# Kernel optimization log

Hardware: AMD Instinct MI355X
Metric: run time of the kernel (lower is better)

## Reference

```python
import jax, jax.numpy as jnp
import numpy as np

N = 50000          # num nodes
E = 800000         # num edges
H, C = 2, 64       # heads, per-head channels (hidden_dim=64)
IN_DIM = 128
EDGE_DIM = 32
NEG_SLOPE = 0.2


def setup_inputs() -> dict:
    key = jax.random.key(0)
    ks = jax.random.split(key, 20)
    s = 0.05
    inp = {
        'x': jax.random.normal(ks[0], (N, IN_DIM), jnp.float32),
        'edge_index': jax.random.randint(ks[1], (2, E), 0, N, jnp.int64),
        'edge_attr': jax.random.normal(ks[2], (E, EDGE_DIM), jnp.float32),
    }
    k = 3
    for l in range(3):
        inp[f'Wl{l}'] = jax.random.normal(ks[k], (IN_DIM, H * C), jnp.float32) * s; k += 1
        inp[f'Wr{l}'] = jax.random.normal(ks[k], (IN_DIM, H * C), jnp.float32) * s; k += 1
        inp[f'We{l}'] = jax.random.normal(ks[k], (EDGE_DIM, H * C), jnp.float32) * s; k += 1
        inp[f'att{l}'] = jax.random.normal(ks[k], (H, C), jnp.float32) * s; k += 1
        inp[f'b{l}'] = jnp.zeros((H * C,), jnp.float32)
    return inp


def gatv2_layer(x, src, dst, edge_attr, Wl, Wr, We, att, b):
    # PyG GATv2Conv (concat=True, share_weights=False):
    #   e_ij = att . LeakyReLU(Wl x_j + Wr x_i + We edge_ij)
    #   alpha = softmax_j over neighborhood of dst i; out_i = sum_j alpha_ij * (Wl x_j)
    xl = (x @ Wl).reshape(-1, H, C)              # [N,H,C] source transform
    xr = (x @ Wr).reshape(-1, H, C)              # [N,H,C] target transform
    ea = (edge_attr @ We).reshape(-1, H, C)      # [E,H,C]
    xj = xl[src]                                 # [E,H,C] gather source
    e = jax.nn.leaky_relu(xj + xr[dst] + ea, NEG_SLOPE)
    logits = jnp.einsum('ehc,hc->eh', e, att)    # [E,H]
    # segment softmax over dst neighborhoods
    m = jax.ops.segment_max(logits, dst, num_segments=N)  # [N,H]
    m = jnp.where(jnp.isfinite(m), m, 0.0)
    ex = jnp.exp(logits - m[dst])
    denom = jax.ops.segment_sum(ex, dst, num_segments=N)  # [N,H]
    alpha = ex / (denom[dst] + 1e-16)            # [E,H]
    out = jax.ops.segment_sum(alpha[:, :, None] * xj, dst, num_segments=N)  # [N,H,C]
    return out.reshape(-1, H * C) + b


def reference(x, edge_index, edge_attr,
              Wl0, Wr0, We0, att0, b0,
              Wl1, Wr1, We1, att1, b1,
              Wl2, Wr2, We2, att2, b2):
    src, dst = edge_index[0], edge_index[1]
    h = gatv2_layer(x, src, dst, edge_attr, Wl0, Wr0, We0, att0, b0)
    h = jax.nn.relu(h)
    h = gatv2_layer(h, src, dst, edge_attr, Wl1, Wr1, We1, att1, b1)
    h = jax.nn.relu(h)
    h = gatv2_layer(h, src, dst, edge_attr, Wl2, Wr2, We2, att2, b2)
    return h
```

## Files before the change

### kernel.cpp

```cpp
#include <hip/hip_runtime.h>

typedef unsigned int u32;
typedef unsigned short u16;
typedef __attribute__((ext_vector_type(8))) short bf16x8;
typedef __attribute__((ext_vector_type(4))) float f32x4;

__device__ __forceinline__ u16 f2b(float f){
  u32 x = __float_as_uint(f);
  u32 r = (x + 0x7fffu + ((x >> 16) & 1u)) >> 16;
  return (u16)r;
}
__device__ __forceinline__ float b2f(u16 h){ return __uint_as_float((u32)h << 16); }
__device__ __forceinline__ float bl(u32 u){ return __uint_as_float(u << 16); }
__device__ __forceinline__ float bh(u32 u){ return __uint_as_float(u & 0xffff0000u); }


__global__ void k_detect(const u32* __restrict__ ei, int n, u32* __restrict__ flag){
  int t = blockIdx.x * blockDim.x + threadIdx.x;
  u32 v = 0;
  if (t < n) v = ei[2 * t + 1];
  unsigned long long b = __ballot(v != 0u);
  if ((threadIdx.x & 63) == 0 && b) atomicOr(flag, 1u);
}

__global__ void k_convhist(const int* __restrict__ ei, int* __restrict__ src, int* __restrict__ dst,
                           int* __restrict__ deg, const float* __restrict__ eattr,
                           u16* __restrict__ ea2, int E, const u32* __restrict__ flag){
  int e = blockIdx.x * blockDim.x + threadIdx.x;
  if (e >= E) return;
  bool is64 = (*flag == 0u);
  int s, d;
  if (is64){ s = ei[2 * e]; d = ei[2 * (E + e)]; }
  else     { s = ei[e];     d = ei[E + e]; }
  src[e] = s; dst[e] = d;
  atomicAdd(&deg[d], 1);
  const float4* srow = (const float4*)(eattr + (size_t)e * 32);
  u32 pk[16];
  #pragma unroll
  for (int i = 0; i < 8; i++){
    float4 v = srow[i];
    pk[2*i]   = (u32)f2b(v.x) | ((u32)f2b(v.y) << 16);
    pk[2*i+1] = (u32)f2b(v.z) | ((u32)f2b(v.w) << 16);
  }
  uint4* drow = (uint4*)(ea2 + (size_t)e * 32);
  drow[0] = make_uint4(pk[0], pk[1], pk[2], pk[3]);
  drow[1] = make_uint4(pk[4], pk[5], pk[6], pk[7]);
  drow[2] = make_uint4(pk[8], pk[9], pk[10], pk[11]);
  drow[3] = make_uint4(pk[12], pk[13], pk[14], pk[15]);
}

__global__ __launch_bounds__(256) void k_scan1(const int* __restrict__ deg, int* __restrict__ bsum, int n){
  int b = blockIdx.x, t = threadIdx.x, lane = t & 63, wv = t >> 6;
  int i0 = b * 1024 + t * 4;
  int4 v = make_int4(0,0,0,0);
  if (i0 + 3 < n) v = *(const int4*)(deg + i0);
  else { if (i0 < n) v.x = deg[i0]; if (i0+1 < n) v.y = deg[i0+1]; if (i0+2 < n) v.z = deg[i0+2]; }
  int s = v.x + v.y + v.z + v.w;
  #pragma unroll
  for (int off = 1; off < 64; off <<= 1) s += __shfl_xor(s, off);
  __shared__ int ws[4];
  if (lane == 0) ws[wv] = s;
  __syncthreads();
  if (t == 0) bsum[b] = ws[0] + ws[1] + ws[2] + ws[3];
}

__global__ __launch_bounds__(1024) void k_scan2(int* __restrict__ bsum, int nb, int* __restrict__ segN){
  int t = threadIdx.x, lane = t & 63, w = t >> 6;
  int v = (t < nb) ? bsum[t] : 0;
  int x = v;
  #pragma unroll
  for (int off = 1; off < 64; off <<= 1){
    int y = __shfl_up(x, off);
    if (lane >= off) x += y;
  }
  __shared__ int wsum[16];
  if (lane == 63) wsum[w] = x;
  __syncthreads();
  if (w == 0 && lane < 16){
    int sv = wsum[lane];
    #pragma unroll
    for (int off = 1; off < 16; off <<= 1){
      int y = __shfl_up(sv, off);
      if (lane >= off) sv += y;
    }
    wsum[lane] = sv;
  }
  __syncthreads();
  int woff = (w > 0) ? wsum[w - 1] : 0;
  if (t < nb) bsum[t] = woff + x - v;
  if (t == 0) *segN = wsum[15];
}

__global__ __launch_bounds__(256) void k_scan3(const int* __restrict__ deg, const int* __restrict__ bsum,
                                               int* __restrict__ seg, int n){
  int b = blockIdx.x, t = threadIdx.x, lane = t & 63, wv = t >> 6;
  int i0 = b * 1024 + t * 4;
  int4 v = make_int4(0,0,0,0);
  if (i0 + 3 < n) v = *(const int4*)(deg + i0);
  else { if (i0 < n) v.x = deg[i0]; if (i0+1 < n) v.y = deg[i0+1]; if (i0+2 < n) v.z = deg[i0+2]; }
  int s = v.x + v.y + v.z + v.w;
  int x = s;
  #pragma unroll
  for (int off = 1; off < 64; off <<= 1){
    int y = __shfl_up(x, off);
    if (lane >= off) x += y;
  }
  __shared__ int ws[4];
  if (lane == 63) ws[wv] = x;
  __syncthreads();
  int woff = 0;
  #pragma unroll
  for (int k = 0; k < 4; k++) if (k < wv) woff += ws[k];
  int base = bsum[b] + woff + (x - s);
  if (i0 < n)     seg[i0]     = base;
  if (i0+1 < n)   seg[i0+1]   = base + v.x;
  if (i0+2 < n)   seg[i0+2]   = base + v.x + v.y;
  if (i0+3 < n)   seg[i0+3]   = base + v.x + v.y + v.z;
}

__global__ void k_scatter(const int* __restrict__ src, const int* __restrict__ dst,
                          const int* __restrict__ seg, int* __restrict__ cur,
                          int* __restrict__ ssrc, int* __restrict__ sdst,
                          int* __restrict__ seid, int E){
  int e = blockIdx.x * blockDim.x + threadIdx.x;
  if (e >= E) return;
  int d = dst[e];
  int pos = seg[d] + atomicAdd(&cur[d], 1);
  ssrc[pos] = src[e];
  sdst[pos] = d;
  seid[pos] = e;
}

__global__ __launch_bounds__(256) void k_prepw(
    const float* __restrict__ W0, const float* __restrict__ W1, const float* __restrict__ W2,
    const float* __restrict__ W3, const float* __restrict__ W4, const float* __restrict__ W5,
    u16* __restrict__ WtH, u16* __restrict__ WtL)
{
  int mat = blockIdx.z;
  const float* W = (mat == 0) ? W0 : (mat == 1) ? W1 : (mat == 2) ? W2 :
                   (mat == 3) ? W3 : (mat == 4) ? W4 : W5;
  __shared__ float tile[32][33];
  int kt = blockIdx.x * 32, ct = blockIdx.y * 32;
  int tr = threadIdx.x & 31, ti = threadIdx.x >> 5;
  #pragma unroll
  for (int j = 0; j < 4; j++){
    int kk = ti + 8 * j;
    tile[kk][tr] = W[(size_t)(kt + kk) * 128 + ct + tr];
  }
  __syncthreads();
  #pragma unroll
  for (int j = 0; j < 4; j++){
    int cc = ti + 8 * j;
    float v = tile[tr][cc];
    u16 hi = f2b(v);
    u16 lo = f2b(v - b2f(hi));
    size_t o = (size_t)mat * 16384 + (size_t)(ct + cc) * 128 + kt + tr;
    WtH[o] = hi;
    WtL[o] = lo;
  }
}

__global__ __launch_bounds__(256) void k_gemm2(
    const float* __restrict__ A,
    const u16* __restrict__ WtH, const u16* __restrict__ WtL,
    u16* __restrict__ xlb, u16* __restrict__ xrb, int nrows)
{
  __shared__ u16 sAH[64][72], sAL[64][72];
  __shared__ u16 sWH[128][72], sWL[128][72];
  int t = threadIdx.x, wv = t >> 6, lane = t & 63;
  int col = lane & 15, kg = lane >> 4;
  int r0 = blockIdx.x * 64;
  int mat = blockIdx.y;
  const u16* WHb = WtH + (size_t)mat * 16384;
  const u16* WLb = WtL + (size_t)mat * 16384;

  f32x4 acc[4][2];
  #pragma unroll
  for (int m = 0; m < 4; m++)
    #pragma unroll
    for (int n = 0; n < 2; n++)
      acc[m][n] = (f32x4){0.f, 0.f, 0.f, 0.f};

  int ar = t >> 2, ak = (t & 3) << 4;
  int wc = t >> 1, wk = (t & 1) << 5;

  for (int kh = 0; kh < 2; kh++){
    __syncthreads();
    {
      int gr = r0 + ar;
      const float* ap = A + (size_t)gr * 128 + kh * 64 + ak;
      float4 va = {0,0,0,0}, vb = {0,0,0,0}, vc = {0,0,0,0}, vd = {0,0,0,0};
      if (gr < nrows){
        va = *(const float4*)ap; vb = *(const float4*)(ap + 4);
        vc = *(const float4*)(ap + 8); vd = *(const float4*)(ap + 12);
      }
      float fv[16] = { va.x, va.y, va.z, va.w, vb.x, vb.y, vb.z, vb.w,
                       vc.x, vc.y, vc.z, vc.w, vd.x, vd.y, vd.z, vd.w };
      u32 hp[8], lp[8];
      #pragma unroll
      for (int i = 0; i < 8; i++){
        u16 h0 = f2b(fv[2*i]),   h1 = f2b(fv[2*i+1]);
        u16 l0 = f2b(fv[2*i]   - b2f(h0));
        u16 l1 = f2b(fv[2*i+1] - b2f(h1));
        hp[i] = (u32)h0 | ((u32)h1 << 16);
        lp[i] = (u32)l0 | ((u32)l1 << 16);
      }
      *(uint4*)&sAH[ar][ak]     = make_uint4(hp[0], hp[1], hp[2], hp[3]);
      *(uint4*)&sAH[ar][ak + 8] = make_uint4(hp[4], hp[5], hp[6], hp[7]);
      *(uint4*)&sAL[ar][ak]     = make_uint4(lp[0], lp[1], lp[2], lp[3]);
      *(uint4*)&sAL[ar][ak + 8] = make_uint4(lp[4], lp[5], lp[6], lp[7]);
    }
    {
      const u16* gh = WHb + (size_t)wc * 128 + kh * 64 + wk;
      const u16* gl = WLb + (size_t)wc * 128 + kh * 64 + wk;
      uint4 h0 = *(const uint4*)gh, h1 = *(const uint4*)(gh + 8);
      uint4 h2 = *(const uint4*)(gh + 16), h3 = *(const uint4*)(gh + 24);
      uint4 l0 = *(const uint4*)gl, l1 = *(const uint4*)(gl + 8);
      uint4 l2 = *(const uint4*)(gl + 16), l3 = *(const uint4*)(gl + 24);
      *(uint4*)&sWH[wc][wk]      = h0; *(uint4*)&sWH[wc][wk + 8]  = h1;
      *(uint4*)&sWH[wc][wk + 16] = h2; *(uint4*)&sWH[wc][wk + 24] = h3;
      *(uint4*)&sWL[wc][wk]      = l0; *(uint4*)&sWL[wc][wk + 8]  = l1;
      *(uint4*)&sWL[wc][wk + 16] = l2; *(uint4*)&sWL[wc][wk + 24] = l3;
    }
    __syncthreads();
    #pragma unroll
    for (int ks = 0; ks < 2; ks++){
      bf16x8 bhi0 = *(const bf16x8*)&sWH[wv*32 + col]     [ks*32 + kg*8];
      bf16x8 bhi1 = *(const bf16x8*)&sWH[wv*32 + 16 + col][ks*32 + kg*8];
      bf16x8 blo0 = *(const bf16x8*)&sWL[wv*32 + col]     [ks*32 + kg*8];
      bf16x8 blo1 = *(const bf16x8*)&sWL[wv*32 + 16 + col][ks*32 + kg*8];
      #pragma unroll
      for (int m = 0; m < 4; m++){
        bf16x8 ahv = *(const bf16x8*)&sAH[m*16 + col][ks*32 + kg*8];
        bf16x8 alv = *(const bf16x8*)&sAL[m*16 + col][ks*32 + kg*8];
        acc[m][0] = __builtin_amdgcn_mfma_f32_16x16x32_bf16(ahv, bhi0, acc[m][0], 0, 0, 0);
        acc[m][0] = __builtin_amdgcn_mfma_f32_16x16x32_bf16(alv, bhi0, acc[m][0], 0, 0, 0);
        acc[m][0] = __builtin_amdgcn_mfma_f32_16x16x32_bf16(ahv, blo0, acc[m][0], 0, 0, 0);
        acc[m][1] = __builtin_amdgcn_mfma_f32_16x16x32_bf16(ahv, bhi1, acc[m][1], 0, 0, 0);
        acc[m][1] = __builtin_amdgcn_mfma_f32_16x16x32_bf16(alv, bhi1, acc[m][1], 0, 0, 0);
        acc[m][1] = __builtin_amdgcn_mfma_f32_16x16x32_bf16(ahv, blo1, acc[m][1], 0, 0, 0);
      }
    }
  }
  u16* ob = mat ? xrb : xlb;
  #pragma unroll
  for (int m = 0; m < 4; m++){
    #pragma unroll
    for (int n = 0; n < 2; n++){
      #pragma unroll
      for (int r = 0; r < 4; r++){
        int row = r0 + m*16 + kg*4 + r;
        int c   = wv*32 + n*16 + col;
        if (row < nrows) ob[(size_t)row * 128 + c] = f2b(acc[m][n][r]);
      }
    }
  }
}

__global__ __launch_bounds__(256) void k_edge(
    const int* __restrict__ ssrc, const int* __restrict__ sdst, const int* __restrict__ seid,
    const u16* __restrict__ ea2,
    const u16* __restrict__ xlb, const u16* __restrict__ xrb,
    const float* __restrict__ We, const float* __restrict__ att,
    float2* __restrict__ pr2, int ntiles, int E)
{
  __shared__ float sD[4][16][132];
  int wv = threadIdx.x >> 6, lane = threadIdx.x & 63;
  int col = lane & 15, kg = lane >> 4;
  int er = lane >> 2, q = lane & 3;

  bf16x8 bw[8];
  #pragma unroll
  for (int c = 0; c < 8; c++)
    #pragma unroll
    for (int j = 0; j < 8; j++)
      bw[c][j] = (short)f2b(We[(kg * 8 + j) * 128 + c * 16 + col]);
  u32 attp[16];
  #pragma unroll
  for (int i = 0; i < 16; i++)
    attp[i] = (u32)f2b(att[q * 32 + 2*i]) | ((u32)f2b(att[q * 32 + 2*i + 1]) << 16);

  int nw = gridDim.x * 4;
  int t = blockIdx.x * 4 + wv;
  if (t >= ntiles) return;

  int e0 = t * 16;
  int eidv = seid[e0 + col];
  bf16x8 a = *(const bf16x8*)(ea2 + (size_t)eidv * 32 + kg * 8);
  int p = e0 + er;
  int sn = ssrc[p], dn = sdst[p];
  const u16* xjp = xlb + (size_t)sn * 128 + q * 32;
  const u16* xip = xrb + (size_t)dn * 128 + q * 32;
  uint4 j0 = ((const uint4*)xjp)[0], j1 = ((const uint4*)xjp)[1],
        j2 = ((const uint4*)xjp)[2], j3 = ((const uint4*)xjp)[3];
  uint4 i0 = ((const uint4*)xip)[0], i1 = ((const uint4*)xip)[1],
        i2 = ((const uint4*)xip)[2], i3 = ((const uint4*)xip)[3];

  while (true){
    int t2 = t + nw;
    bool more = (t2 < ntiles);
    int tc = more ? t2 : t;
    int e02 = tc * 16;
    int p2 = e02 + er;
    int sn2 = ssrc[p2], dn2 = sdst[p2];
    int eid2 = seid[e02 + col];
    bf16x8 a2 = *(const bf16x8*)(ea2 + (size_t)eid2 * 32 + kg * 8);

    #pragma unroll
    for (int c = 0; c < 8; c++){
      f32x4 d = __builtin_amdgcn_mfma_f32_16x16x32_bf16(a, bw[c], (f32x4){0.f,0.f,0.f,0.f}, 0, 0, 0);
      #pragma unroll
      for (int r = 0; r < 4; r++)
        sD[wv][kg * 4 + r][c * 16 + col] = d[r];
    }

    const u16* xj2 = xlb + (size_t)sn2 * 128 + q * 32;
    const u16* xi2 = xrb + (size_t)dn2 * 128 + q * 32;
    uint4 nj0 = ((const uint4*)xj2)[0], nj1 = ((const uint4*)xj2)[1],
          nj2 = ((const uint4*)xj2)[2], nj3 = ((const uint4*)xj2)[3];
    uint4 ni0 = ((const uint4*)xi2)[0], ni1 = ((const uint4*)xi2)[1],
          ni2 = ((const uint4*)xi2)[2], ni3 = ((const uint4*)xi2)[3];

    const float* drow = &sD[wv][er][q * 32];
    float acc = 0.f;
#define EPK(KO, JQ, IQ) { \
    float4 d0 = *(const float4*)(drow + KO*8); \
    float4 d1 = *(const float4*)(drow + KO*8 + 4); \
    float v; u32 jw, iw, aw; \
    jw = JQ.x; iw = IQ.x; aw = attp[KO*4+0]; \
    v = d0.x + bl(jw) + bl(iw); v = fmaxf(v, 0.2f*v); acc = fmaf(v, bl(aw), acc); \
    v = d0.y + bh(jw) + bh(iw); v = fmaxf(v, 0.2f*v); acc = fmaf(v, bh(aw), acc); \
    jw = JQ.y; iw = IQ.y; aw = attp[KO*4+1]; \
    v = d0.z + bl(jw) + bl(iw); v = fmaxf(v, 0.2f*v); acc = fmaf(v, bl(aw), acc); \
    v = d0.w + bh(jw) + bh(iw); v = fmaxf(v, 0.2f*v); acc = fmaf(v, bh(aw), acc); \
    jw = JQ.z; iw = IQ.z; aw = attp[KO*4+2]; \
    v = d1.x + bl(jw) + bl(iw); v = fmaxf(v, 0.2f*v); acc = fmaf(v, bl(aw), acc); \
    v = d1.y + bh(jw) + bh(iw); v = fmaxf(v, 0.2f*v); acc = fmaf(v, bh(aw), acc); \
    jw = JQ.w; iw = IQ.w; aw = attp[KO*4+3]; \
    v = d1.z + bl(jw) + bl(iw); v = fmaxf(v, 0.2f*v); acc = fmaf(v, bl(aw), acc); \
    v = d1.w + bh(jw) + bh(iw); v = fmaxf(v, 0.2f*v); acc = fmaf(v, bh(aw), acc); }
    EPK(0, j0, i0) EPK(1, j1, i1) EPK(2, j2, i2) EPK(3, j3, i3)
#undef EPK
    acc += __shfl_xor(acc, 1);
    float other = __shfl_xor(acc, 2);
    if (q == 0 && p < E){
      pr2[p] = make_float2(__expf(fminf(acc, 80.f)), __expf(fminf(other, 80.f)));
    }
    if (!more) break;
    t = t2; p = p2; a = a2;
    j0 = nj0; j1 = nj1; j2 = nj2; j3 = nj3;
    i0 = ni0; i1 = ni1; i2 = ni2; i3 = ni3;
  }
}

template<int RELU>
__global__ __launch_bounds__(256) void k_seg2(
    const int* __restrict__ seg, const int* __restrict__ ssrc,
    const float2* __restrict__ pr2,
    const u16* __restrict__ xlb, const float* __restrict__ bias,
    float* __restrict__ out, int N)
{
  int wid  = blockIdx.x * 4 + (threadIdx.x >> 6);
  int lane = threadIdx.x & 63;
  if (wid >= N) return;
  int c0 = lane * 2, head = lane >> 5;

  int p0 = seg[wid], p1 = seg[wid + 1];
  float2 bv = *(const float2*)(bias + c0);
  float s = 0.f, o0 = 0.f, o1 = 0.f;

  if (p0 < p1){
#define LDB(K, PP, QN, XN) \
    { int ii = (PP + K < p1) ? (PP + K) : (p1 - 1); \
      int ss = ssrc[ii]; \
      QN = pr2[ii]; \
      XN = *(const u32*)(xlb + (size_t)ss * 128 + c0); }
    float2 qa0, qa1, qa2, qa3, qa4, qa5, qa6, qa7;
    u32 xa0, xa1, xa2, xa3, xa4, xa5, xa6, xa7;
    LDB(0, p0, qa0, xa0) LDB(1, p0, qa1, xa1) LDB(2, p0, qa2, xa2) LDB(3, p0, qa3, xa3)
    LDB(4, p0, qa4, xa4) LDB(5, p0, qa5, xa5) LDB(6, p0, qa6, xa6) LDB(7, p0, qa7, xa7)
    int p = p0;
    while (true){
      int pn = p + 8;
      bool more = pn < p1;
      int pc = more ? pn : p;
      float2 qb0, qb1, qb2, qb3, qb4, qb5, qb6, qb7;
      u32 xb0, xb1, xb2, xb3, xb4, xb5, xb6, xb7;
      LDB(0, pc, qb0, xb0) LDB(1, pc, qb1, xb1) LDB(2, pc, qb2, xb2) LDB(3, pc, qb3, xb3)
      LDB(4, pc, qb4, xb4) LDB(5, pc, qb5, xb5) LDB(6, pc, qb6, xb6) LDB(7, pc, qb7, xb7)
#define ACC(K, QN, XN) { \
      float e = head ? QN.y : QN.x; \
      if (p + K >= p1) e = 0.f; \
      s += e; \
      o0 = fmaf(e, bl(XN), o0); \
      o1 = fmaf(e, bh(XN), o1); }
      ACC(0, qa0, xa0) ACC(1, qa1, xa1) ACC(2, qa2, xa2) ACC(3, qa3, xa3)
      ACC(4, qa4, xa4) ACC(5, qa5, xa5) ACC(6, qa6, xa6) ACC(7, qa7, xa7)
#undef ACC
      if (!more) break;
      p = pn;
      qa0 = qb0; xa0 = xb0; qa1 = qb1; xa1 = xb1;
      qa2 = qb2; xa2 = xb2; qa3 = qb3; xa3 = xb3;
      qa4 = qb4; xa4 = xb4; qa5 = qb5; xa5 = xb5;
      qa6 = qb6; xa6 = xb6; qa7 = qb7; xa7 = xb7;
    }
#undef LDB
  }
  float inv = 1.0f / (s + 1e-16f);
  float r0 = fmaf(o0, inv, bv.x);
  float r1 = fmaf(o1, inv, bv.y);
  if (RELU){ r0 = fmaxf(r0, 0.f); r1 = fmaxf(r1, 0.f); }
  *(float2*)(out + (size_t)wid * 128 + c0) = make_float2(r0, r1);
}

extern "C" void kernel_launch(void* const* d_in, const int* in_sizes, int n_in,
                              void* d_out, int out_size, void* d_ws, size_t ws_size,
                              hipStream_t stream)
{
  const float* x     = (const float*)d_in[0];
  const int*   ei    = (const int*)  d_in[1];
  const float* eattr = (const float*)d_in[2];
  const float* Wp[3][5];
  for (int l = 0; l < 3; l++)
    for (int j = 0; j < 5; j++)
      Wp[l][j] = (const float*)d_in[3 + l * 5 + j];

  int N = in_sizes[0] / 128;
  int E = in_sizes[2] / 32;

  char* w = (char*)d_ws;
  auto alloc = [&](size_t bytes) -> char* {
    char* p = w; w += (bytes + 255) & ~(size_t)255; return p;
  };
  float* xr   = (float*)alloc((size_t)N * 128 * 4);
  u16*   xlb  = (u16*)  alloc((size_t)N * 128 * 2);
  u16*   xrb  = (u16*)  alloc((size_t)N * 128 * 2);
  u16*   ea2  = (u16*)  alloc((size_t)(E + 64) * 32 * 2);
  float2* prb = (float2*)alloc((size_t)E * 8);
  u16*   WtH  = (u16*)  alloc((size_t)6 * 16384 * 2);
  u16*   WtL  = (u16*)  alloc((size_t)6 * 16384 * 2);
  int* srcA   = (int*)alloc((size_t)E * 4);
  int* dstA   = (int*)alloc((size_t)E * 4);
  int* ssrc   = (int*)alloc((size_t)(E + 64) * 4);
  int* sdst   = (int*)alloc((size_t)(E + 64) * 4);
  int* seid   = (int*)alloc((size_t)(E + 64) * 4);
  int* deg    = (int*)alloc((size_t)N * 4);
  int* cur    = (int*)alloc((size_t)N * 4);
  int* seg    = (int*)alloc((size_t)(N + 1) * 4);
  int* bsum   = (int*)alloc(1024 * 4);
  u32* flag   = (u32*)alloc(256);

  hipMemsetAsync(deg,  0, (size_t)N * 4, stream);
  hipMemsetAsync(cur,  0, (size_t)N * 4, stream);
  hipMemsetAsync(flag, 0, 4, stream);
  hipMemsetAsync(ssrc + E, 0, 64 * 4, stream);
  hipMemsetAsync(sdst + E, 0, 64 * 4, stream);
  hipMemsetAsync(seid + E, 0, 64 * 4, stream);

  int ndet = (E < 16384) ? E : 16384;
  k_detect<<<(ndet + 255) / 256, 256, 0, stream>>>((const u32*)ei, ndet, flag);
  int gE = (E + 255) / 256;
  k_convhist<<<gE, 256, 0, stream>>>(ei, srcA, dstA, deg, eattr, ea2, E, flag);
  int nb = (N + 1023) / 1024;
  k_scan1<<<nb, 256, 0, stream>>>(deg, bsum, N);
  k_scan2<<<1, 1024, 0, stream>>>(bsum, nb, seg + N);
  k_scan3<<<nb, 256, 0, stream>>>(deg, bsum, seg, N);
  k_scatter<<<gE, 256, 0, stream>>>(srcA, dstA, seg, cur, ssrc, sdst, seid, E);
  dim3 gp(4, 4, 6);
  k_prepw<<<gp, 256, 0, stream>>>(Wp[0][0], Wp[0][1], Wp[1][0], Wp[1][1], Wp[2][0], Wp[2][1], WtH, WtL);

  int gS = (N + 3) / 4;
  int ntiles = (E + 15) / 16;
  int gEdge = (ntiles + 3) / 4; if (gEdge > 2048) gEdge = 2048;
  dim3 gG2((N + 63) / 64, 2);

  const float* hin = x;
  for (int l = 0; l < 3; l++){
    k_gemm2<<<gG2, 256, 0, stream>>>(hin, WtH + (size_t)l * 2 * 16384, WtL + (size_t)l * 2 * 16384, xlb, xrb, N);
    k_edge<<<gEdge, 256, 0, stream>>>(ssrc, sdst, seid, ea2, xlb, xrb, Wp[l][2], Wp[l][3], prb, ntiles, E);
    float* outp = (l == 2) ? (float*)d_out : xr;
    if (l == 2) k_seg2<0><<<gS, 256, 0, stream>>>(seg, ssrc, prb, xlb, Wp[l][4], outp, N);
    else        k_seg2<1><<<gS, 256, 0, stream>>>(seg, ssrc, prb, xlb, Wp[l][4], outp, N);
    hin = xr;
  }
}
```

Measured before the change: 538.4 us.

## Compute edge attention logits directly in MFMA output layout without LDS staging

The edge kernel now swaps the MFMA operands so each lane holds a transposed accumulator slice (one edge per column, four channels per lane). It gathers the matching xl/xr channels as small uint2 loads and computes the LeakyReLU-attention dot product in registers. This removes the shared-memory round trip through sD and its write/read traffic. The cost is more, narrower gather loads per lane (8-byte instead of 16-byte chunks) and a cross-lane shuffle reduction over 16 and 32.

```diff
diff --git a/kernel.cpp b/kernel.cpp
--- a/kernel.cpp
+++ b/kernel.cpp
@@ -264,21 +264,19 @@
     const float* __restrict__ We, const float* __restrict__ att,
     float2* __restrict__ pr2, int ntiles, int E)
 {
-  __shared__ float sD[4][16][132];
   int wv = threadIdx.x >> 6, lane = threadIdx.x & 63;
   int col = lane & 15, kg = lane >> 4;
-  int er = lane >> 2, q = lane & 3;
-
-  bf16x8 bw[8];
-  #pragma unroll
-  for (int c = 0; c < 8; c++)
-    #pragma unroll
-    for (int j = 0; j < 8; j++)
-      bw[c][j] = (short)f2b(We[(kg * 8 + j) * 128 + c * 16 + col]);
-  u32 attp[16];
-  #pragma unroll
-  for (int i = 0; i < 16; i++)
-    attp[i] = (u32)f2b(att[q * 32 + 2*i]) | ((u32)f2b(att[q * 32 + 2*i + 1]) << 16);
+
+#define LDWE(C) bf16x8 bw##C; { \
+    _Pragma("unroll") \
+    for (int j = 0; j < 8; j++) bw##C[j] = (short)f2b(We[(kg * 8 + j) * 128 + C * 16 + col]); }
+  LDWE(0) LDWE(1) LDWE(2) LDWE(3) LDWE(4) LDWE(5) LDWE(6) LDWE(7)
+#undef LDWE
+#define LDAT(C) \
+  u32 al##C = (u32)f2b(att[C*16 + kg*4])     | ((u32)f2b(att[C*16 + kg*4 + 1]) << 16); \
+  u32 ah##C = (u32)f2b(att[C*16 + kg*4 + 2]) | ((u32)f2b(att[C*16 + kg*4 + 3]) << 16);
+  LDAT(0) LDAT(1) LDAT(2) LDAT(3) LDAT(4) LDAT(5) LDAT(6) LDAT(7)
+#undef LDAT
 
   int nw = gridDim.x * 4;
   int t = blockIdx.x * 4 + wv;
@@ -286,71 +284,63 @@
 
   int e0 = t * 16;
   int eidv = seid[e0 + col];
+  int sn = ssrc[e0 + col], dn = sdst[e0 + col];
   bf16x8 a = *(const bf16x8*)(ea2 + (size_t)eidv * 32 + kg * 8);
-  int p = e0 + er;
-  int sn = ssrc[p], dn = sdst[p];
-  const u16* xjp = xlb + (size_t)sn * 128 + q * 32;
-  const u16* xip = xrb + (size_t)dn * 128 + q * 32;
-  uint4 j0 = ((const uint4*)xjp)[0], j1 = ((const uint4*)xjp)[1],
-        j2 = ((const uint4*)xjp)[2], j3 = ((const uint4*)xjp)[3];
-  uint4 i0 = ((const uint4*)xip)[0], i1 = ((const uint4*)xip)[1],
-        i2 = ((const uint4*)xip)[2], i3 = ((const uint4*)xip)[3];
+  const u16* xjp = xlb + (size_t)sn * 128 + kg * 4;
+  const u16* xip = xrb + (size_t)dn * 128 + kg * 4;
+#define LDX(C, P, V) uint2 V = *(const uint2*)((P) + (C) * 16);
+  LDX(0, xjp, J0) LDX(1, xjp, J1) LDX(2, xjp, J2) LDX(3, xjp, J3)
+  LDX(4, xjp, J4) LDX(5, xjp, J5) LDX(6, xjp, J6) LDX(7, xjp, J7)
+  LDX(0, xip, I0) LDX(1, xip, I1) LDX(2, xip, I2) LDX(3, xip, I3)
+  LDX(4, xip, I4) LDX(5, xip, I5) LDX(6, xip, I6) LDX(7, xip, I7)
 
   while (true){
     int t2 = t + nw;
     bool more = (t2 < ntiles);
     int tc = more ? t2 : t;
     int e02 = tc * 16;
-    int p2 = e02 + er;
-    int sn2 = ssrc[p2], dn2 = sdst[p2];
     int eid2 = seid[e02 + col];
+    int sn2 = ssrc[e02 + col], dn2 = sdst[e02 + col];
     bf16x8 a2 = *(const bf16x8*)(ea2 + (size_t)eid2 * 32 + kg * 8);
-
-    #pragma unroll
-    for (int c = 0; c < 8; c++){
-      f32x4 d = __builtin_amdgcn_mfma_f32_16x16x32_bf16(a, bw[c], (f32x4){0.f,0.f,0.f,0.f}, 0, 0, 0);
-      #pragma unroll
-      for (int r = 0; r < 4; r++)
-        sD[wv][kg * 4 + r][c * 16 + col] = d[r];
-    }
-
-    const u16* xj2 = xlb + (size_t)sn2 * 128 + q * 32;
-    const u16* xi2 = xrb + (size_t)dn2 * 128 + q * 32;
-    uint4 nj0 = ((const uint4*)xj2)[0], nj1 = ((const uint4*)xj2)[1],
-          nj2 = ((const uint4*)xj2)[2], nj3 = ((const uint4*)xj2)[3];
-    uint4 ni0 = ((const uint4*)xi2)[0], ni1 = ((const uint4*)xi2)[1],
-          ni2 = ((const uint4*)xi2)[2], ni3 = ((const uint4*)xi2)[3];
-
-    const float* drow = &sD[wv][er][q * 32];
-    float acc = 0.f;
-#define EPK(KO, JQ, IQ) { \
-    float4 d0 = *(const float4*)(drow + KO*8); \
-    float4 d1 = *(const float4*)(drow + KO*8 + 4); \
-    float v; u32 jw, iw, aw; \
-    jw = JQ.x; iw = IQ.x; aw = attp[KO*4+0]; \
-    v = d0.x + bl(jw) + bl(iw); v = fmaxf(v, 0.2f*v); acc = fmaf(v, bl(aw), acc); \
-    v = d0.y + bh(jw) + bh(iw); v = fmaxf(v, 0.2f*v); acc = fmaf(v, bh(aw), acc); \
-    jw = JQ.y; iw = IQ.y; aw = attp[KO*4+1]; \
-    v = d0.z + bl(jw) + bl(iw); v = fmaxf(v, 0.2f*v); acc = fmaf(v, bl(aw), acc); \
-    v = d0.w + bh(jw) + bh(iw); v = fmaxf(v, 0.2f*v); acc = fmaf(v, bh(aw), acc); \
-    jw = JQ.z; iw = IQ.z; aw = attp[KO*4+2]; \
-    v = d1.x + bl(jw) + bl(iw); v = fmaxf(v, 0.2f*v); acc = fmaf(v, bl(aw), acc); \
-    v = d1.y + bh(jw) + bh(iw); v = fmaxf(v, 0.2f*v); acc = fmaf(v, bh(aw), acc); \
-    jw = JQ.w; iw = IQ.w; aw = attp[KO*4+3]; \
-    v = d1.z + bl(jw) + bl(iw); v = fmaxf(v, 0.2f*v); acc = fmaf(v, bl(aw), acc); \
-    v = d1.w + bh(jw) + bh(iw); v = fmaxf(v, 0.2f*v); acc = fmaf(v, bh(aw), acc); }
-    EPK(0, j0, i0) EPK(1, j1, i1) EPK(2, j2, i2) EPK(3, j3, i3)
-#undef EPK
-    acc += __shfl_xor(acc, 1);
-    float other = __shfl_xor(acc, 2);
-    if (q == 0 && p < E){
-      pr2[p] = make_float2(__expf(fminf(acc, 80.f)), __expf(fminf(other, 80.f)));
+    const u16* xj2 = xlb + (size_t)sn2 * 128 + kg * 4;
+    const u16* xi2 = xrb + (size_t)dn2 * 128 + kg * 4;
+    LDX(0, xj2, nJ0) LDX(1, xj2, nJ1) LDX(2, xj2, nJ2) LDX(3, xj2, nJ3)
+    LDX(4, xj2, nJ4) LDX(5, xj2, nJ5) LDX(6, xj2, nJ6) LDX(7, xj2, nJ7)
+    LDX(0, xi2, nI0) LDX(1, xi2, nI1) LDX(2, xi2, nI2) LDX(3, xi2, nI3)
+    LDX(4, xi2, nI4) LDX(5, xi2, nI5) LDX(6, xi2, nI6) LDX(7, xi2, nI7)
+
+    f32x4 d0 = __builtin_amdgcn_mfma_f32_16x16x32_bf16(bw0, a, (f32x4){0.f,0.f,0.f,0.f}, 0, 0, 0);
+    f32x4 d1 = __builtin_amdgcn_mfma_f32_16x16x32_bf16(bw1, a, (f32x4){0.f,0.f,0.f,0.f}, 0, 0, 0);
+    f32x4 d2 = __builtin_amdgcn_mfma_f32_16x16x32_bf16(bw2, a, (f32x4){0.f,0.f,0.f,0.f}, 0, 0, 0);
+    f32x4 d3 = __builtin_amdgcn_mfma_f32_16x16x32_bf16(bw3, a, (f32x4){0.f,0.f,0.f,0.f}, 0, 0, 0);
+    f32x4 d4 = __builtin_amdgcn_mfma_f32_16x16x32_bf16(bw4, a, (f32x4){0.f,0.f,0.f,0.f}, 0, 0, 0);
+    f32x4 d5 = __builtin_amdgcn_mfma_f32_16x16x32_bf16(bw5, a, (f32x4){0.f,0.f,0.f,0.f}, 0, 0, 0);
+    f32x4 d6 = __builtin_amdgcn_mfma_f32_16x16x32_bf16(bw6, a, (f32x4){0.f,0.f,0.f,0.f}, 0, 0, 0);
+    f32x4 d7 = __builtin_amdgcn_mfma_f32_16x16x32_bf16(bw7, a, (f32x4){0.f,0.f,0.f,0.f}, 0, 0, 0);
+
+    float h0 = 0.f, h1 = 0.f;
+#define EPC(D, J, I, AL, AH, ACC) { \
+    float v0 = D[0] + bl(J.x) + bl(I.x); v0 = fmaxf(v0, 0.2f*v0); ACC = fmaf(v0, bl(AL), ACC); \
+    float v1 = D[1] + bh(J.x) + bh(I.x); v1 = fmaxf(v1, 0.2f*v1); ACC = fmaf(v1, bh(AL), ACC); \
+    float v2 = D[2] + bl(J.y) + bl(I.y); v2 = fmaxf(v2, 0.2f*v2); ACC = fmaf(v2, bl(AH), ACC); \
+    float v3 = D[3] + bh(J.y) + bh(I.y); v3 = fmaxf(v3, 0.2f*v3); ACC = fmaf(v3, bh(AH), ACC); }
+    EPC(d0, J0, I0, al0, ah0, h0) EPC(d1, J1, I1, al1, ah1, h0)
+    EPC(d2, J2, I2, al2, ah2, h0) EPC(d3, J3, I3, al3, ah3, h0)
+    EPC(d4, J4, I4, al4, ah4, h1) EPC(d5, J5, I5, al5, ah5, h1)
+    EPC(d6, J6, I6, al6, ah6, h1) EPC(d7, J7, I7, al7, ah7, h1)
+#undef EPC
+
+    h0 += __shfl_xor(h0, 16); h0 += __shfl_xor(h0, 32);
+    h1 += __shfl_xor(h1, 16); h1 += __shfl_xor(h1, 32);
+    if (kg == 0 && e0 + col < E){
+      pr2[e0 + col] = make_float2(__expf(fminf(h0, 80.f)), __expf(fminf(h1, 80.f)));
     }
     if (!more) break;
-    t = t2; p = p2; a = a2;
-    j0 = nj0; j1 = nj1; j2 = nj2; j3 = nj3;
-    i0 = ni0; i1 = ni1; i2 = ni2; i3 = ni3;
-  }
+    t = t2; e0 = e02; a = a2;
+    J0 = nJ0; J1 = nJ1; J2 = nJ2; J3 = nJ3; J4 = nJ4; J5 = nJ5; J6 = nJ6; J7 = nJ7;
+    I0 = nI0; I1 = nI1; I2 = nI2; I3 = nI3; I4 = nI4; I5 = nI5; I6 = nI6; I7 = nI7;
+  }
+#undef LDX
 }
 
 template<int RELU>
```

New measurement: 598.3 us. 11.1% more time.
